# Optimization experiments

Measured on AMD Instinct MI355X. Metric: run time of the kernel, lower is better.

The kernel has to match this reference:

```python
import jax, jax.numpy as jnp
import numpy as np

N, E, H = 5000, 40000, 8
DIMS = [(258, 512), (516, 256), (262, 128), (136, 20)]  # (in_feature, out_feature) per GATDeformer


def setup_inputs() -> dict:
    key = jax.random.key(0)
    ks = jax.random.split(key, 10)
    s = 0.05
    data = jax.random.normal(ks[0], (N, 10), jnp.float32)
    src = jax.random.randint(ks[1], (E,), 0, N)
    off = jax.random.randint(ks[2], (E,), 1, N)
    edge_idx = jnp.stack([src, (src + off) % N]).astype(jnp.int32)  # no self loops by construction
    inp = {
        'data': data,
        'edge_idx': edge_idx,
        'W0': jax.random.normal(ks[3], (10, 256), jnp.float32) * s,
        'b0': jnp.zeros((256,), jnp.float32),
    }
    for i, (din, dout) in enumerate(DIMS, start=1):
        k = jax.random.split(ks[3 + i], 3)
        inp[f'W{i}'] = jax.random.normal(k[0], (din, H * dout), jnp.float32) * s
        inp[f'asrc{i}'] = jax.random.normal(k[1], (H, dout), jnp.float32) * s
        inp[f'adst{i}'] = jax.random.normal(k[2], (H, dout), jnp.float32) * s
        inp[f'bias{i}'] = jnp.zeros((dout,), jnp.float32)
    return inp


def _gat(x, src, dst, W, a_s, a_d, b):
    """PyG GATConv (concat=False): returns (mean-over-heads output + bias, alpha [E',H])."""
    Hh, C = a_s.shape
    h = (x @ W).reshape(N, Hh, C)                               # [N,H,C]
    e_s = jnp.einsum('nhc,hc->nh', h, a_s)                      # [N,H]
    e_d = jnp.einsum('nhc,hc->nh', h, a_d)
    logits = jax.nn.leaky_relu(e_s[src] + e_d[dst], 0.2)        # [E',H]
    m = jax.ops.segment_max(logits, dst, num_segments=N)        # segment softmax over incoming edges
    ex = jnp.exp(logits - m[dst])
    alpha = ex / jax.ops.segment_sum(ex, dst, num_segments=N)[dst]
    out = jax.ops.segment_sum(alpha[:, :, None] * h[src], dst, num_segments=N)  # [N,H,C]
    return out.mean(axis=1) + b, alpha


def _deformer(af, src, dst, W, a_s, a_d, b):
    # find_boundary on the layer input features
    up, down = af[:, 0] == 1.0, af[:, 0] == 0.0
    left, right = af[:, 1] == 0.0, af[:, 1] == 1.0
    feat, alpha = _gat(af, src, dst, W, a_s, a_d, b)
    coord = af[:, :2]
    # second propagate: alpha*0.2 reused to aggregate source coordinates, then mean over heads
    msg = (alpha * 0.2)[:, :, None] * coord[src][:, None, :]    # [E',H,2]
    oc = jax.ops.segment_sum(msg, dst, num_segments=N).mean(axis=1)
    # fix_boundary (sequential overwrite order: up then down, left then right)
    c0 = jnp.where(down, 0.0, jnp.where(up, 1.0, oc[:, 0]))
    c1 = jnp.where(right, 1.0, jnp.where(left, 0.0, oc[:, 1]))
    return jnp.stack([c0, c1], axis=1), jax.nn.selu(feat)


def reference(data, edge_idx, W0, b0, W1, asrc1, adst1, bias1, W2, asrc2, adst2, bias2, W3, asrc3, adst3, bias3, W4, asrc4, adst4, bias4):
    sl = jnp.arange(N, dtype=edge_idx.dtype)
    src = jnp.concatenate([edge_idx[0], sl])   # GATConv add_self_loops=True
    dst = jnp.concatenate([edge_idx[1], sl])
    coord = data[:, :2]
    feat = jax.nn.selu(data @ W0 + b0)
    c1_, f1 = _deformer(jnp.concatenate([coord, feat], 1), src, dst, W1, asrc1, adst1, bias1)
    c2_, f2 = _deformer(jnp.concatenate([c1_, coord, f1], 1), src, dst, W2, asrc2, adst2, bias2)
    c3_, f3 = _deformer(jnp.concatenate([c2_, c1_, coord, f2], 1), src, dst, W3, asrc3, adst3, bias3)
    c4_, _ = _deformer(jnp.concatenate([c3_, c2_, c1_, coord, f3], 1), src, dst, W4, asrc4, adst4, bias4)
    return c4_
```

## Files before the change

### kernel.cpp

```cpp
#include <hip/hip_runtime.h>

#define N_NODES 5000
#define NH 8

typedef unsigned short u16;
typedef short bf16x8 __attribute__((ext_vector_type(8)));
typedef float f32x4 __attribute__((ext_vector_type(4)));

static __device__ __forceinline__ float selu_f(float x) {
    const float sc = 1.0507009873554805f;
    const float al = 1.6732632423543772f;
    return x > 0.f ? sc * x : sc * al * (__expf(x) - 1.f);
}

static __device__ __forceinline__ u16 f2bf(float x) {
    union { float f; unsigned u; } v; v.f = x;
    unsigned r = v.u + 0x7fff + ((v.u >> 16) & 1);
    return (u16)(r >> 16);
}

static __device__ __forceinline__ float bf2f(unsigned hi16) {
    union { unsigned u; float f; } v; v.u = hi16 << 16;
    return v.f;
}

#define GL2LDS16(gp, lp)                                                        \
    __builtin_amdgcn_global_load_lds(                                           \
        (const __attribute__((address_space(1))) void*)(gp),                    \
        (__attribute__((address_space(3))) void*)(lp), 16, 0, 0)

#define WAVE_LDS_FENCE() asm volatile("s_waitcnt lgkmcnt(0)" ::: "memory")

__global__ __launch_bounds__(256) void k_prepcs(
        const float* W1, const float* W2, const float* W3, const float* W4,
        const float* s1, const float* s2, const float* s3, const float* s4,
        const float* d1, const float* d2, const float* d3, const float* d4,
        float* __restrict__ fsAll, float* __restrict__ fdAll,
        u16* T1, u16* T2, u16* T3,
        const int* __restrict__ ei, int E,
        int* __restrict__ rowp, int* __restrict__ curp) {
    const int Ks[4] = {258, 516, 262, 136};
    const int Cs[4] = {512, 256, 128, 20};
    __shared__ float tile[32][33];
    __shared__ int hist[N_NODES];
    __shared__ int ps2[256];
    int bid = blockIdx.x;
    if (bid < 516) {
        int li = bid / 129;
        int k = (bid % 129) * 4 + (threadIdx.x >> 6);
        int lane = threadIdx.x & 63;
        if (k >= Ks[li]) return;
        const float* W  = (li == 0) ? W1 : (li == 1) ? W2 : (li == 2) ? W3 : W4;
        const float* as = (li == 0) ? s1 : (li == 1) ? s2 : (li == 2) ? s3 : s4;
        const float* ad = (li == 0) ? d1 : (li == 1) ? d2 : (li == 2) ? d3 : d4;
        int C = Cs[li];
        float s[8] = {0.f,0.f,0.f,0.f,0.f,0.f,0.f,0.f};
        float d[8] = {0.f,0.f,0.f,0.f,0.f,0.f,0.f,0.f};
        const float* wr = W + (size_t)k * 8 * C;
        for (int c = lane; c < C; c += 64) {
            #pragma unroll
            for (int h = 0; h < 8; ++h) {
                float w = wr[h * C + c];
                s[h] += w * as[h * C + c];
                d[h] += w * ad[h * C + c];
            }
        }
        #pragma unroll
        for (int off = 32; off >= 1; off >>= 1) {
            #pragma unroll
            for (int h = 0; h < 8; ++h) {
                s[h] += __shfl_xor(s[h], off);
                d[h] += __shfl_xor(d[h], off);
            }
        }
        if (lane == 0) {
            float* fo = fsAll + (size_t)li * 516 * 8 + k * 8;
            float* go = fdAll + (size_t)li * 516 * 8 + k * 8;
            #pragma unroll
            for (int h = 0; h < 8; ++h) { fo[h] = s[h]; go[h] = d[h]; }
        }
    } else if (bid < 7044) {
        const int Kps[3] = {288, 544, 288};
        int w = bid - 516;
        int li = w / (16 * 136);
        int rem = w % (16 * 136);
        int c0 = (rem % 16) * 32;
        int j0 = (rem / 16) * 32;
        int C = Cs[li], K = Ks[li], Kp = Kps[li], KK = 8 * Kp;
        if (c0 >= C || j0 >= KK) return;
        const float* W = (li == 0) ? W1 : (li == 1) ? W2 : W3;
        u16* Wt2 = (li == 0) ? T1 : (li == 1) ? T2 : T3;
        int h = j0 / Kp, k0 = j0 % Kp;
        int tid = threadIdx.x;
        for (int idx = tid; idx < 1024; idx += 256) {
            int kr = idx >> 5, cc = idx & 31;
            int gk = k0 + kr;
            tile[kr][cc] = (gk < K) ? W[(size_t)gk * (8 * C) + h * C + c0 + cc] : 0.f;
        }
        __syncthreads();
        for (int idx = tid; idx < 1024; idx += 256) {
            int cr = idx >> 5, kc = idx & 31;
            Wt2[(size_t)(c0 + cr) * KK + j0 + kc] = f2bf(tile[kc][cr]);
        }
    } else {
        int t = threadIdx.x;
        for (int i = t; i < N_NODES; i += 256) hist[i] = 1;
        __syncthreads();
        for (int e = t; e < E; e += 256) atomicAdd(&hist[ei[E + e]], 1);
        __syncthreads();
        int per = (N_NODES + 255) / 256;
        int b = t * per;
        int s = 0;
        for (int i = 0; i < per; ++i) { int idx = b + i; if (idx < N_NODES) s += hist[idx]; }
        ps2[t] = s;
        __syncthreads();
        for (int off = 1; off < 256; off <<= 1) {
            int v = (t >= off) ? ps2[t - off] : 0;
            __syncthreads();
            ps2[t] += v;
            __syncthreads();
        }
        int run = (t == 0) ? 0 : ps2[t - 1];
        for (int i = 0; i < per; ++i) {
            int idx = b + i;
            if (idx < N_NODES) { rowp[idx] = run; run += hist[idx]; }
        }
        if (t == 255) rowp[N_NODES] = run;
        for (int i = t; i < N_NODES; i += 256) curp[i] = 0;
    }
}

__global__ __launch_bounds__(256) void k_fmf1(
        const int* __restrict__ ei, const int* __restrict__ rowp,
        int* __restrict__ curp, int* __restrict__ ssrc, int E, int Esz, int gE,
        const float* __restrict__ data, const float* __restrict__ W0,
        const float* __restrict__ b0,
        const float* __restrict__ fs, const float* __restrict__ fd,
        u16* __restrict__ afb, float* __restrict__ es, float* __restrict__ ed,
        float* __restrict__ c0out) {
    int bid = blockIdx.x, t = threadIdx.x;
    if (bid < gE) {
        int e = bid * 256 + t;
        if (e >= Esz) return;
        int src, dst;
        if (e < E) { src = ei[e]; dst = ei[E + e]; }
        else       { src = e - E; dst = src; }
        int pos = rowp[dst] + atomicAdd(&curp[dst], 1);
        ssrc[pos] = src;
        return;
    }
    const int FC = 256, K = 258, Kp = 288;
    int n = bid - gE;
    __shared__ float drow[10];
    if (t < 10) drow[t] = data[n * 10 + t];
    __syncthreads();
    float pes[8] = {0.f,0.f,0.f,0.f,0.f,0.f,0.f,0.f};
    float ped[8] = {0.f,0.f,0.f,0.f,0.f,0.f,0.f,0.f};
    u16* rowb = afb + (size_t)n * Kp;
    for (int cf2 = t; 2 * cf2 < FC; cf2 += 256) {
        int cf = 2 * cf2;
        float2 bb = *(const float2*)(b0 + cf);
        float v0 = bb.x, v1 = bb.y;
        #pragma unroll
        for (int k = 0; k < 10; ++k) {
            float2 ww = *(const float2*)(W0 + k * 256 + cf);
            v0 += drow[k] * ww.x;
            v1 += drow[k] * ww.y;
        }
        v0 = selu_f(v0); v1 = selu_f(v1);
        int c = 2 + cf;
        *(unsigned*)(rowb + c) = (unsigned)f2bf(v0) | ((unsigned)f2bf(v1) << 16);
        const float* fsr = fs + c * 8;
        const float* fdr = fd + c * 8;
        #pragma unroll
        for (int h = 0; h < 8; ++h) {
            pes[h] += v0 * fsr[h] + v1 * fsr[8 + h];
            ped[h] += v0 * fdr[h] + v1 * fdr[8 + h];
        }
    }
    if (t < 2) {
        float v = drow[t];
        c0out[n * 2 + t] = v;
        rowb[t] = f2bf(v);
        #pragma unroll
        for (int h = 0; h < 8; ++h) { pes[h] += v * fs[t * 8 + h]; ped[h] += v * fd[t * 8 + h]; }
    }
    for (int c = K + t; c < Kp; c += 256) rowb[c] = 0;
    #pragma unroll
    for (int off = 32; off >= 1; off >>= 1) {
        #pragma unroll
        for (int h = 0; h < 8; ++h) {
            pes[h] += __shfl_xor(pes[h], off);
            ped[h] += __shfl_xor(ped[h], off);
        }
    }
    __shared__ float red[4][16];
    int wv = t >> 6, ln = t & 63;
    if (ln == 0) {
        #pragma unroll
        for (int h = 0; h < 8; ++h) { red[wv][h] = pes[h]; red[wv][8 + h] = ped[h]; }
    }
    __syncthreads();
    if (t < 16) {
        float s = red[0][t] + red[1][t] + red[2][t] + red[3][t];
        if (t < 8) es[n * 8 + t] = s;
        else       ed[n * 8 + (t - 8)] = s;
    }
}

__global__ __launch_bounds__(256) void k_mf(const float* p0, const float* p1,
                                            const float* p2, const float* p3, int np,
                                            const u16* __restrict__ facc,
                                            const float* __restrict__ biasp,
                                            int split, int MN, int FC, int K, int Kp,
                                            const float* __restrict__ fs,
                                            const float* __restrict__ fd,
                                            u16* __restrict__ afb,
                                            float* __restrict__ es, float* __restrict__ ed) {
    int n = blockIdx.x, t = threadIdx.x;
    float pes[8] = {0.f,0.f,0.f,0.f,0.f,0.f,0.f,0.f};
    float ped[8] = {0.f,0.f,0.f,0.f,0.f,0.f,0.f,0.f};
    u16* rowb = afb + (size_t)n * Kp;
    for (int cf2 = t; 2 * cf2 < FC; cf2 += 256) {
        int cf = 2 * cf2;
        float s0 = 0.f, s1 = 0.f;
        for (int z = 0; z < split; ++z) {
            unsigned pr = *(const unsigned*)(facc + (size_t)z * MN + (size_t)n * FC + cf);
            s0 += bf2f(pr & 0xffff);
            s1 += bf2f(pr >> 16);
        }
        float2 bb = *(const float2*)(biasp + cf);
        float v0 = selu_f(s0 * 0.125f + bb.x);
        float v1 = selu_f(s1 * 0.125f + bb.y);
        int c = 2 * np + cf;
        *(unsigned*)(rowb + c) = (unsigned)f2bf(v0) | ((unsigned)f2bf(v1) << 16);
        const float* fsr = fs + c * 8;
        const float* fdr = fd + c * 8;
        #pragma unroll
        for (int h = 0; h < 8; ++h) {
            pes[h] += v0 * fsr[h] + v1 * fsr[8 + h];
            ped[h] += v0 * fdr[h] + v1 * fdr[8 + h];
        }
    }
    if (t < 2 * np) {
        const float* p = (t < 2) ? p0 : (t < 4) ? p1 : (t < 6) ? p2 : p3;
        float v = p[n * 2 + (t & 1)];
        rowb[t] = f2bf(v);
        #pragma unroll
        for (int h = 0; h < 8; ++h) { pes[h] += v * fs[t * 8 + h]; ped[h] += v * fd[t * 8 + h]; }
    }
    for (int c = K + t; c < Kp; c += 256) rowb[c] = 0;
    #pragma unroll
    for (int off = 32; off >= 1; off >>= 1) {
        #pragma unroll
        for (int h = 0; h < 8; ++h) {
            pes[h] += __shfl_xor(pes[h], off);
            ped[h] += __shfl_xor(ped[h], off);
        }
    }
    __shared__ float red[4][16];
    int wv = t >> 6, ln = t & 63;
    if (ln == 0) {
        #pragma unroll
        for (int h = 0; h < 8; ++h) { red[wv][h] = pes[h]; red[wv][8 + h] = ped[h]; }
    }
    __syncthreads();
    if (t < 16) {
        float s = red[0][t] + red[1][t] + red[2][t] + red[3][t];
        if (t < 8) es[n * 8 + t] = s;
        else       ed[n * 8 + (t - 8)] = s;
    }
}

template <int S>
__global__ __launch_bounds__(256) void k_gag2(const float* __restrict__ es,
                            const float* __restrict__ ed,
                            const int* __restrict__ rowp, const int* __restrict__ ssrc,
                            const float* __restrict__ cprev, const u16* __restrict__ afb,
                            u16* __restrict__ g, float* __restrict__ cnext, int Kp) {
    __shared__ float la_s[4][128 * 8];
    __shared__ int   ls_s[4][128];
    __shared__ float linv_s[4][8];
    int w4 = threadIdx.x >> 6, lane = threadIdx.x & 63;
    int n = blockIdx.x * 4 + w4;
    if (n >= N_NODES) return;
    float* la = la_s[w4];
    int*   ls = ls_s[w4];
    float* linv = linv_s[w4];

    int s0 = rowp[n];
    int deg = rowp[n + 1] - s0;
    if (deg > 128) deg = 128;
    for (int i = lane; i < deg; i += 64) ls[i] = ssrc[s0 + i];
    WAVE_LDS_FENCE();

    int h = lane & 7, ei = lane >> 3;
    float edh = ed[n * 8 + h];
    float m = -1e30f;
    for (int b = 0; b < deg; b += 8) {
        int e = b + ei;
        if (e < deg) {
            float x = es[ls[e] * 8 + h] + edh;
            x = x > 0.f ? x : 0.2f * x;
            la[e * 8 + h] = x;
            m = fmaxf(m, x);
        }
    }
    m = fmaxf(m, __shfl_xor(m, 8));
    m = fmaxf(m, __shfl_xor(m, 16));
    m = fmaxf(m, __shfl_xor(m, 32));
    WAVE_LDS_FENCE();
    float ssum = 0.f;
    for (int b = 0; b < deg; b += 8) {
        int e = b + ei;
        if (e < deg) {
            float v = __expf(la[e * 8 + h] - m);
            la[e * 8 + h] = v;
            ssum += v;
        }
    }
    ssum += __shfl_xor(ssum, 8);
    ssum += __shfl_xor(ssum, 16);
    ssum += __shfl_xor(ssum, 32);
    if (lane < 8) linv[lane] = 1.f / ssum;
    WAVE_LDS_FENCE();

    int nW = Kp >> 1;
    float linv8[8];
    #pragma unroll
    for (int h2 = 0; h2 < 8; ++h2) linv8[h2] = linv[h2];

    float acc[8][2 * S];
    #pragma unroll
    for (int h2 = 0; h2 < 8; ++h2)
        #pragma unroll
        for (int s = 0; s < 2 * S; ++s) acc[h2][s] = 0.f;
    int e = 0;
    for (; e + 3 < deg; e += 4) {
        const unsigned* r0 = (const unsigned*)(afb + (size_t)ls[e] * Kp);
        const unsigned* r1 = (const unsigned*)(afb + (size_t)ls[e + 1] * Kp);
        const unsigned* r2 = (const unsigned*)(afb + (size_t)ls[e + 2] * Kp);
        const unsigned* r3 = (const unsigned*)(afb + (size_t)ls[e + 3] * Kp);
        unsigned v0[S], v1[S], v2[S], v3[S];
        #pragma unroll
        for (int s = 0; s < S; ++s) {
            int w = lane + 64 * s;
            bool ok = (w < nW);
            v0[s] = ok ? r0[w] : 0u;
            v1[s] = ok ? r1[w] : 0u;
            v2[s] = ok ? r2[w] : 0u;
            v3[s] = ok ? r3[w] : 0u;
        }
        float a0[8], a1[8], a2[8], a3[8];
        #pragma unroll
        for (int h2 = 0; h2 < 8; ++h2) {
            a0[h2] = la[(e + 0) * 8 + h2];
            a1[h2] = la[(e + 1) * 8 + h2];
            a2[h2] = la[(e + 2) * 8 + h2];
            a3[h2] = la[(e + 3) * 8 + h2];
        }
        #pragma unroll
        for (int s = 0; s < S; ++s) {
            float x0 = bf2f(v0[s] & 0xffff), y0 = bf2f(v0[s] >> 16);
            float x1 = bf2f(v1[s] & 0xffff), y1 = bf2f(v1[s] >> 16);
            float x2 = bf2f(v2[s] & 0xffff), y2 = bf2f(v2[s] >> 16);
            float x3 = bf2f(v3[s] & 0xffff), y3 = bf2f(v3[s] >> 16);
            #pragma unroll
            for (int h2 = 0; h2 < 8; ++h2) {
                acc[h2][2 * s]     += a0[h2] * x0 + a1[h2] * x1 + a2[h2] * x2 + a3[h2] * x3;
                acc[h2][2 * s + 1] += a0[h2] * y0 + a1[h2] * y1 + a2[h2] * y2 + a3[h2] * y3;
            }
        }
    }
    for (; e < deg; ++e) {
        const unsigned* r0 = (const unsigned*)(afb + (size_t)ls[e] * Kp);
        unsigned v0[S];
        #pragma unroll
        for (int s = 0; s < S; ++s) {
            int w = lane + 64 * s;
            v0[s] = (w < nW) ? r0[w] : 0u;
        }
        float a0[8];
        #pragma unroll
        for (int h2 = 0; h2 < 8; ++h2) a0[h2] = la[e * 8 + h2];
        #pragma unroll
        for (int s = 0; s < S; ++s) {
            float x0 = bf2f(v0[s] & 0xffff), y0 = bf2f(v0[s] >> 16);
            #pragma unroll
            for (int h2 = 0; h2 < 8; ++h2) {
                acc[h2][2 * s]     += a0[h2] * x0;
                acc[h2][2 * s + 1] += a0[h2] * y0;
            }
        }
    }
    unsigned* grw = (unsigned*)(g + (size_t)n * 8 * Kp);
    #pragma unroll
    for (int s = 0; s < S; ++s) {
        int w = lane + 64 * s;
        if (w < nW) {
            #pragma unroll
            for (int h2 = 0; h2 < 8; ++h2) {
                float iv = linv8[h2];
                unsigned lo = f2bf(acc[h2][2 * s] * iv);
                unsigned hi = f2bf(acc[h2][2 * s + 1] * iv);
                grw[h2 * nW + w] = lo | (hi << 16);
            }
        }
    }
    float oc0 = 0.f, oc1 = 0.f;
    for (int i = lane; i < deg; i += 64) {
        float wsum = 0.f;
        #pragma unroll
        for (int h2 = 0; h2 < 8; ++h2) wsum += la[i * 8 + h2] * linv8[h2];
        int src = ls[i];
        oc0 += wsum * cprev[src * 2];
        oc1 += wsum * cprev[src * 2 + 1];
    }
    #pragma unroll
    for (int off = 1; off <= 32; off <<= 1) {
        oc0 += __shfl_xor(oc0, off);
        oc1 += __shfl_xor(oc1, off);
    }
    if (lane == 0) {
        oc0 *= 0.025f; oc1 *= 0.025f;
        float a0 = cprev[n * 2], a1 = cprev[n * 2 + 1];
        cnext[n * 2]     = (a0 == 0.f) ? 0.f : ((a0 == 1.f) ? 1.f : oc0);
        cnext[n * 2 + 1] = (a1 == 1.f) ? 1.f : ((a1 == 0.f) ? 0.f : oc1);
    }
}

__global__ __launch_bounds__(256) void k_gemm_s(const u16* __restrict__ A,
                                                const u16* __restrict__ Bt,
                                                u16* __restrict__ facc16,
                                                int M, int KK, int NC, int kchunk, int MN) {
    __shared__ u16 As[3][128 * 32];
    __shared__ u16 Bs[3][128 * 32];
    int tid = threadIdx.x;
    int wave = tid >> 6, lane = tid & 63;
    int bm = blockIdx.y * 128, bn = blockIdx.x * 128, z = blockIdx.z;
    int kbeg = z * kchunk, kend = min(KK, kbeg + kchunk);
    int wm = (wave >> 1) * 64, wn = (wave & 1) * 64;
    int l16 = lane & 15, q = lane >> 4;
    f32x4 acc[4][4] = {};

    int seg0 = wave * 128 + lane;
    int seg1 = seg0 + 64;
    int row0 = seg0 >> 2, sq0 = (seg0 & 3) ^ (row0 & 3);
    int row1 = seg1 >> 2, sq1 = (seg1 & 3) ^ (row1 & 3);
    const u16* ga0 = A  + (size_t)(bm + row0) * KK + sq0 * 8;
    const u16* ga1 = A  + (size_t)(bm + row1) * KK + sq1 * 8;
    const u16* gb0 = Bt + (size_t)(bn + row0) * KK + sq0 * 8;
    const u16* gb1 = Bt + (size_t)(bn + row1) * KK + sq1 * 8;
    int lo0 = (wave * 2 + 0) * 512;
    int lo1 = (wave * 2 + 1) * 512;

#define STAGE_T(buf, kk)                          \
    do {                                          \
        GL2LDS16(ga0 + (kk), &As[buf][lo0]);      \
        GL2LDS16(ga1 + (kk), &As[buf][lo1]);      \
        GL2LDS16(gb0 + (kk), &Bs[buf][lo0]);      \
        GL2LDS16(gb1 + (kk), &Bs[buf][lo1]);      \
    } while (0)

    STAGE_T(0, kbeg);
    if (kbeg + 32 < kend) STAGE_T(1, kbeg + 32);
    int cur = 0;
    for (int k0 = kbeg; k0 < kend; k0 += 32) {
        if (k0 + 64 < kend) {
            int nb = cur + 2; if (nb >= 3) nb -= 3;
            STAGE_T(nb, k0 + 64);
            asm volatile("s_waitcnt vmcnt(8)" ::: "memory");
        } else if (k0 + 32 < kend) {
            asm volatile("s_waitcnt vmcnt(4)" ::: "memory");
        } else {
            asm volatile("s_waitcnt vmcnt(0)" ::: "memory");
        }
        __builtin_amdgcn_s_barrier();
        const u16* Asr = As[cur];
        const u16* Bsr = Bs[cur];
        bf16x8 fa[4], fb[4];
        #pragma unroll
        for (int mi = 0; mi < 4; ++mi) {
            int row = wm + mi * 16 + l16;
            fa[mi] = *(const bf16x8*)(Asr + row * 32 + ((q ^ (row & 3)) * 8));
            int col = wn + mi * 16 + l16;
            fb[mi] = *(const bf16x8*)(Bsr + col * 32 + ((q ^ (col & 3)) * 8));
        }
        #pragma unroll
        for (int mi = 0; mi < 4; ++mi)
            #pragma unroll
            for (int ni = 0; ni < 4; ++ni)
                acc[mi][ni] = __builtin_amdgcn_mfma_f32_16x16x32_bf16(fa[mi], fb[ni], acc[mi][ni], 0, 0, 0);
        __builtin_amdgcn_s_barrier();
        cur += 1; if (cur >= 3) cur -= 3;
    }
#undef STAGE_T
    u16* out = facc16 + (size_t)z * MN;
    #pragma unroll
    for (int mi = 0; mi < 4; ++mi) {
        int row0s = bm + wm + mi * 16 + q * 4;
        #pragma unroll
        for (int ni = 0; ni < 4; ++ni) {
            int col = bn + wn + ni * 16 + l16;
            #pragma unroll
            for (int r = 0; r < 4; ++r) {
                int row = row0s + r;
                if (row < M) out[(size_t)row * NC + col] = f2bf(acc[mi][ni][r]);
            }
        }
    }
}

__global__ void k_final(const float* __restrict__ es, const float* __restrict__ ed,
                        const int* __restrict__ rowp, const int* __restrict__ ssrc,
                        const float* __restrict__ cprev, float* __restrict__ outp) {
    int wid = (blockIdx.x * blockDim.x + threadIdx.x) >> 6;
    int lane = threadIdx.x & 63;
    if (wid >= N_NODES) return;
    int n = wid;
    int s0 = rowp[n], deg = rowp[n + 1] - s0;
    int h = lane & 7, ei = lane >> 3;
    float edh = ed[n * 8 + h];
    float m = -1e30f;
    for (int b = 0; b < deg; b += 8) {
        int e = b + ei;
        if (e < deg) {
            int src = ssrc[s0 + e];
            float x = es[src * 8 + h] + edh;
            x = x > 0.f ? x : 0.2f * x;
            m = fmaxf(m, x);
        }
    }
    m = fmaxf(m, __shfl_xor(m, 8));
    m = fmaxf(m, __shfl_xor(m, 16));
    m = fmaxf(m, __shfl_xor(m, 32));
    float ssum = 0.f;
    for (int b = 0; b < deg; b += 8) {
        int e = b + ei;
        if (e < deg) {
            int src = ssrc[s0 + e];
            float x = es[src * 8 + h] + edh;
            x = x > 0.f ? x : 0.2f * x;
            ssum += __expf(x - m);
        }
    }
    ssum += __shfl_xor(ssum, 8);
    ssum += __shfl_xor(ssum, 16);
    ssum += __shfl_xor(ssum, 32);
    float inv = 1.f / ssum;
    float oc0 = 0.f, oc1 = 0.f;
    for (int b = 0; b < deg; b += 8) {
        int e = b + ei;
        if (e < deg) {
            int src = ssrc[s0 + e];
            float x = es[src * 8 + h] + edh;
            x = x > 0.f ? x : 0.2f * x;
            float w = __expf(x - m) * inv;
            w += __shfl_xor(w, 1);
            w += __shfl_xor(w, 2);
            w += __shfl_xor(w, 4);
            if (h == 0) {
                oc0 += w * cprev[src * 2];
                oc1 += w * cprev[src * 2 + 1];
            }
        }
    }
    oc0 += __shfl_xor(oc0, 8);  oc1 += __shfl_xor(oc1, 8);
    oc0 += __shfl_xor(oc0, 16); oc1 += __shfl_xor(oc1, 16);
    oc0 += __shfl_xor(oc0, 32); oc1 += __shfl_xor(oc1, 32);
    if (lane == 0) {
        oc0 *= 0.025f; oc1 *= 0.025f;
        float a0 = cprev[n * 2], a1 = cprev[n * 2 + 1];
        outp[n * 2]     = (a0 == 0.f) ? 0.f : ((a0 == 1.f) ? 1.f : oc0);
        outp[n * 2 + 1] = (a1 == 1.f) ? 1.f : ((a1 == 0.f) ? 0.f : oc1);
    }
}

extern "C" void kernel_launch(void* const* d_in, const int* in_sizes, int n_in,
                              void* d_out, int out_size, void* d_ws, size_t ws_size,
                              hipStream_t stream) {
    const float* data = (const float*)d_in[0];
    const int* ei = (const int*)d_in[1];
    const float* W0 = (const float*)d_in[2];
    const float* b0 = (const float*)d_in[3];
    int E = in_sizes[1] / 2;
    int Esz = E + N_NODES;
    int gE = (Esz + 255) / 256;

    char* wp = (char*)d_ws;
    size_t off = 0;
    auto alloc = [&](size_t bytes) {
        void* p = wp + off;
        off += (bytes + 1023) & ~(size_t)1023;
        return p;
    };
    u16*   g     = (u16*)alloc((size_t)N_NODES * 8 * 576 * 2);
    u16*   T1    = (u16*)alloc((size_t)512 * 8 * 288 * 2);
    u16*   T2    = (u16*)alloc((size_t)256 * 8 * 544 * 2);
    u16*   T3    = (u16*)alloc((size_t)128 * 8 * 288 * 2);
    u16*   facc  = (u16*)alloc((size_t)8 * N_NODES * 512 * 2);
    u16*   afb   = (u16*)alloc((size_t)N_NODES * 576 * 2);
    float* es    = (float*)alloc((size_t)N_NODES * 8 * 4);
    float* ebd   = (float*)alloc((size_t)N_NODES * 8 * 4);
    float* fsAll = (float*)alloc((size_t)4 * 516 * 8 * 4);
    float* fdAll = (float*)alloc((size_t)4 * 516 * 8 * 4);
    float* c0    = (float*)alloc(N_NODES * 2 * 4);
    float* c1    = (float*)alloc(N_NODES * 2 * 4);
    float* c2    = (float*)alloc(N_NODES * 2 * 4);
    float* c3    = (float*)alloc(N_NODES * 2 * 4);
    int* cur  = (int*)alloc(N_NODES * 4);
    int* rowp = (int*)alloc((N_NODES + 1) * 4);
    int* ssrc = (int*)alloc(Esz * 4);

    struct LP { const float *W, *as, *ad, *bs; int K, C, split; };
    LP L[4] = {
        {(const float*)d_in[4],  (const float*)d_in[5],  (const float*)d_in[6],  (const float*)d_in[7],  258, 512, 4},
        {(const float*)d_in[8],  (const float*)d_in[9],  (const float*)d_in[10], (const float*)d_in[11], 516, 256, 8},
        {(const float*)d_in[12], (const float*)d_in[13], (const float*)d_in[14], (const float*)d_in[15], 262, 128, 8},
        {(const float*)d_in[16], (const float*)d_in[17], (const float*)d_in[18], (const float*)d_in[19], 136, 20, 1},
    };

    k_prepcs<<<7045, 256, 0, stream>>>(
        L[0].W, L[1].W, L[2].W, L[3].W,
        L[0].as, L[1].as, L[2].as, L[3].as,
        L[0].ad, L[1].ad, L[2].ad, L[3].ad,
        fsAll, fdAll, T1, T2, T3,
        ei, E, rowp, cur);

    k_fmf1<<<gE + N_NODES, 256, 0, stream>>>(
        ei, rowp, cur, ssrc, E, Esz, gE,
        data, W0, b0,
        fsAll + 0, fdAll + 0, afb, es, ebd, c0);

    float* cbuf[4] = {c0, c1, c2, c3};
    u16* Tb[3] = {T1, T2, T3};
    int FC[4] = {256, 512, 256, 128};

    for (int li = 0; li < 4; ++li) {
        LP& lp = L[li];
        int Kp = ((lp.K + 31) / 32) * 32;
        int KK = 8 * Kp;

        if (li >= 1) {
            const float* p[4] = {nullptr, nullptr, nullptr, nullptr};
            for (int j = 0; j <= li; ++j) p[j] = cbuf[li - j];
            const float* biasp = L[li - 1].bs;
            int splitp = L[li - 1].split;
            int MNp = N_NODES * FC[li];
            const float* fs = fsAll + (size_t)li * 516 * 8;
            const float* fd = fdAll + (size_t)li * 516 * 8;
            k_mf<<<N_NODES, 256, 0, stream>>>(p[0], p[1], p[2], p[3], li + 1,
                                              facc, biasp, splitp, MNp, FC[li],
                                              lp.K, Kp, fs, fd, afb, es, ebd);
        }
        if (li < 3) {
            int gG = (N_NODES + 3) / 4;
            if (Kp == 544)
                k_gag2<5><<<gG, 256, 0, stream>>>(es, ebd, rowp, ssrc, cbuf[li], afb,
                                                  g, cbuf[li + 1], Kp);
            else
                k_gag2<3><<<gG, 256, 0, stream>>>(es, ebd, rowp, ssrc, cbuf[li], afb,
                                                  g, cbuf[li + 1], Kp);
            int MN = N_NODES * lp.C;
            k_gemm_s<<<dim3(lp.C / 128, (N_NODES + 127) / 128, lp.split), 256, 0, stream>>>(
                g, Tb[li], facc, N_NODES, KK, lp.C, KK / lp.split, MN);
        } else {
            k_final<<<(N_NODES + 3) / 4, 256, 0, stream>>>(es, ebd, rowp, ssrc, cbuf[3],
                                                           (float*)d_out);
        }
    }
}
```

Before: 374.1 us.

## Replace CSR build with fixed-capacity per-node adjacency buckets

Removes the single-block histogram and prefix-scan that built CSR row pointers inside the prep kernel. Edges are now placed directly into a padded per-destination bucket of MAXDEG slots through an atomic counter, and the gather and final kernels read the count and bucket row instead of rowp/ssrc. This takes a serial, one-workgroup scan off the critical path, at the cost of a larger sparse adjacency buffer. Nodes with degree above MAXDEG are silently truncated, which the old code also did in the gather kernel but not in the final kernel.

```diff
diff --git a/kernel.cpp b/kernel.cpp
--- a/kernel.cpp
+++ b/kernel.cpp
@@ -2,6 +2,7 @@
 
 #define N_NODES 5000
 #define NH 8
+#define MAXDEG 128
 
 typedef unsigned short u16;
 typedef short bf16x8 __attribute__((ext_vector_type(8)));
@@ -31,19 +32,14 @@
 
 #define WAVE_LDS_FENCE() asm volatile("s_waitcnt lgkmcnt(0)" ::: "memory")
 
-__global__ __launch_bounds__(256) void k_prepcs(
+__global__ __launch_bounds__(256) void k_prep(
         const float* W1, const float* W2, const float* W3, const float* W4,
         const float* s1, const float* s2, const float* s3, const float* s4,
         const float* d1, const float* d2, const float* d3, const float* d4,
         float* __restrict__ fsAll, float* __restrict__ fdAll,
-        u16* T1, u16* T2, u16* T3,
-        const int* __restrict__ ei, int E,
-        int* __restrict__ rowp, int* __restrict__ curp) {
+        u16* T1, u16* T2, u16* T3, int* __restrict__ cnt) {
     const int Ks[4] = {258, 516, 262, 136};
     const int Cs[4] = {512, 256, 128, 20};
-    __shared__ float tile[32][33];
-    __shared__ int hist[N_NODES];
-    __shared__ int ps2[256];
     int bid = blockIdx.x;
     if (bid < 516) {
         int li = bid / 129;
@@ -90,6 +86,7 @@
         if (c0 >= C || j0 >= KK) return;
         const float* W = (li == 0) ? W1 : (li == 1) ? W2 : W3;
         u16* Wt2 = (li == 0) ? T1 : (li == 1) ? T2 : T3;
+        __shared__ float tile[32][33];
         int h = j0 / Kp, k0 = j0 % Kp;
         int tid = threadIdx.x;
         for (int idx = tid; idx < 1024; idx += 256) {
@@ -103,36 +100,13 @@
             Wt2[(size_t)(c0 + cr) * KK + j0 + kc] = f2bf(tile[kc][cr]);
         }
     } else {
-        int t = threadIdx.x;
-        for (int i = t; i < N_NODES; i += 256) hist[i] = 1;
-        __syncthreads();
-        for (int e = t; e < E; e += 256) atomicAdd(&hist[ei[E + e]], 1);
-        __syncthreads();
-        int per = (N_NODES + 255) / 256;
-        int b = t * per;
-        int s = 0;
-        for (int i = 0; i < per; ++i) { int idx = b + i; if (idx < N_NODES) s += hist[idx]; }
-        ps2[t] = s;
-        __syncthreads();
-        for (int off = 1; off < 256; off <<= 1) {
-            int v = (t >= off) ? ps2[t - off] : 0;
-            __syncthreads();
-            ps2[t] += v;
-            __syncthreads();
-        }
-        int run = (t == 0) ? 0 : ps2[t - 1];
-        for (int i = 0; i < per; ++i) {
-            int idx = b + i;
-            if (idx < N_NODES) { rowp[idx] = run; run += hist[idx]; }
-        }
-        if (t == 255) rowp[N_NODES] = run;
-        for (int i = t; i < N_NODES; i += 256) curp[i] = 0;
-    }
-}
-
-__global__ __launch_bounds__(256) void k_fmf1(
-        const int* __restrict__ ei, const int* __restrict__ rowp,
-        int* __restrict__ curp, int* __restrict__ ssrc, int E, int Esz, int gE,
+        for (int i = threadIdx.x; i < N_NODES; i += 256) cnt[i] = 0;
+    }
+}
+
+__global__ __launch_bounds__(256) void k_fmf1b(
+        const int* __restrict__ ei, int* __restrict__ cnt,
+        int* __restrict__ ssrcb, int E, int Esz, int gE,
         const float* __restrict__ data, const float* __restrict__ W0,
         const float* __restrict__ b0,
         const float* __restrict__ fs, const float* __restrict__ fd,
@@ -145,8 +119,8 @@
         int src, dst;
         if (e < E) { src = ei[e]; dst = ei[E + e]; }
         else       { src = e - E; dst = src; }
-        int pos = rowp[dst] + atomicAdd(&curp[dst], 1);
-        ssrc[pos] = src;
+        int pos = atomicAdd(&cnt[dst], 1);
+        if (pos < MAXDEG) ssrcb[dst * MAXDEG + pos] = src;
         return;
     }
     const int FC = 256, K = 258, Kp = 288;
@@ -275,7 +249,7 @@
 template <int S>
 __global__ __launch_bounds__(256) void k_gag2(const float* __restrict__ es,
                             const float* __restrict__ ed,
-                            const int* __restrict__ rowp, const int* __restrict__ ssrc,
+                            const int* __restrict__ cnt, const int* __restrict__ ssrcb,
                             const float* __restrict__ cprev, const u16* __restrict__ afb,
                             u16* __restrict__ g, float* __restrict__ cnext, int Kp) {
     __shared__ float la_s[4][128 * 8];
@@ -288,10 +262,10 @@
     int*   ls = ls_s[w4];
     float* linv = linv_s[w4];
 
-    int s0 = rowp[n];
-    int deg = rowp[n + 1] - s0;
-    if (deg > 128) deg = 128;
-    for (int i = lane; i < deg; i += 64) ls[i] = ssrc[s0 + i];
+    int deg = cnt[n];
+    if (deg > MAXDEG) deg = MAXDEG;
+    const int* row = ssrcb + (size_t)n * MAXDEG;
+    for (int i = lane; i < deg; i += 64) ls[i] = row[i];
     WAVE_LDS_FENCE();
 
     int h = lane & 7, ei = lane >> 3;
@@ -512,20 +486,22 @@
 }
 
 __global__ void k_final(const float* __restrict__ es, const float* __restrict__ ed,
-                        const int* __restrict__ rowp, const int* __restrict__ ssrc,
+                        const int* __restrict__ cnt, const int* __restrict__ ssrcb,
                         const float* __restrict__ cprev, float* __restrict__ outp) {
     int wid = (blockIdx.x * blockDim.x + threadIdx.x) >> 6;
     int lane = threadIdx.x & 63;
     if (wid >= N_NODES) return;
     int n = wid;
-    int s0 = rowp[n], deg = rowp[n + 1] - s0;
+    int deg = cnt[n];
+    if (deg > MAXDEG) deg = MAXDEG;
+    const int* row = ssrcb + (size_t)n * MAXDEG;
     int h = lane & 7, ei = lane >> 3;
     float edh = ed[n * 8 + h];
     float m = -1e30f;
     for (int b = 0; b < deg; b += 8) {
         int e = b + ei;
         if (e < deg) {
-            int src = ssrc[s0 + e];
+            int src = row[e];
             float x = es[src * 8 + h] + edh;
             x = x > 0.f ? x : 0.2f * x;
             m = fmaxf(m, x);
@@ -538,7 +514,7 @@
     for (int b = 0; b < deg; b += 8) {
         int e = b + ei;
         if (e < deg) {
-            int src = ssrc[s0 + e];
+            int src = row[e];
             float x = es[src * 8 + h] + edh;
             x = x > 0.f ? x : 0.2f * x;
             ssum += __expf(x - m);
@@ -552,7 +528,7 @@
     for (int b = 0; b < deg; b += 8) {
         int e = b + ei;
         if (e < deg) {
-            int src = ssrc[s0 + e];
+            int src = row[e];
             float x = es[src * 8 + h] + edh;
             x = x > 0.f ? x : 0.2f * x;
             float w = __expf(x - m) * inv;
@@ -608,9 +584,8 @@
     float* c1    = (float*)alloc(N_NODES * 2 * 4);
     float* c2    = (float*)alloc(N_NODES * 2 * 4);
     float* c3    = (float*)alloc(N_NODES * 2 * 4);
-    int* cur  = (int*)alloc(N_NODES * 4);
-    int* rowp = (int*)alloc((N_NODES + 1) * 4);
-    int* ssrc = (int*)alloc(Esz * 4);
+    int* cnt   = (int*)alloc(N_NODES * 4);
+    int* ssrcb = (int*)alloc((size_t)N_NODES * MAXDEG * 4);
 
     struct LP { const float *W, *as, *ad, *bs; int K, C, split; };
     LP L[4] = {
@@ -620,15 +595,14 @@
         {(const float*)d_in[16], (const float*)d_in[17], (const float*)d_in[18], (const float*)d_in[19], 136, 20, 1},
     };
 
-    k_prepcs<<<7045, 256, 0, stream>>>(
+    k_prep<<<7045, 256, 0, stream>>>(
         L[0].W, L[1].W, L[2].W, L[3].W,
         L[0].as, L[1].as, L[2].as, L[3].as,
         L[0].ad, L[1].ad, L[2].ad, L[3].ad,
-        fsAll, fdAll, T1, T2, T3,
-        ei, E, rowp, cur);
-
-    k_fmf1<<<gE + N_NODES, 256, 0, stream>>>(
-        ei, rowp, cur, ssrc, E, Esz, gE,
+        fsAll, fdAll, T1, T2, T3, cnt);
+
+    k_fmf1b<<<gE + N_NODES, 256, 0, stream>>>(
+        ei, cnt, ssrcb, E, Esz, gE,
         data, W0, b0,
         fsAll + 0, fdAll + 0, afb, es, ebd, c0);
 
@@ -656,16 +630,16 @@
         if (li < 3) {
             int gG = (N_NODES + 3) / 4;
             if (Kp == 544)
-                k_gag2<5><<<gG, 256, 0, stream>>>(es, ebd, rowp, ssrc, cbuf[li], afb,
+                k_gag2<5><<<gG, 256, 0, stream>>>(es, ebd, cnt, ssrcb, cbuf[li], afb,
                                                   g, cbuf[li + 1], Kp);
             else
-                k_gag2<3><<<gG, 256, 0, stream>>>(es, ebd, rowp, ssrc, cbuf[li], afb,
+                k_gag2<3><<<gG, 256, 0, stream>>>(es, ebd, cnt, ssrcb, cbuf[li], afb,
                                                   g, cbuf[li + 1], Kp);
             int MN = N_NODES * lp.C;
             k_gemm_s<<<dim3(lp.C / 128, (N_NODES + 127) / 128, lp.split), 256, 0, stream>>>(
                 g, Tb[li], facc, N_NODES, KK, lp.C, KK / lp.split, MN);
         } else {
-            k_final<<<(N_NODES + 3) / 4, 256, 0, stream>>>(es, ebd, rowp, ssrc, cbuf[3],
+            k_final<<<(N_NODES + 3) / 4, 256, 0, stream>>>(es, ebd, cnt, ssrcb, cbuf[3],
                                                            (float*)d_out);
         }
     }
```

Result: faster. 333.2 us (-11.0%).
